# Performance work log

Hardware: AMD Instinct MI355X
Metric: run time of the kernel (lower is better)

## Reference

```python
import jax, jax.numpy as jnp
import numpy as np

B, D_IN, D_HID, D_OUT, E = 8192, 1024, 4096, 1024, 8


def setup_inputs() -> dict:
    key = jax.random.key(0)
    ks = jax.random.split(key, 6)
    s_in = 1.0 / np.sqrt(D_IN)
    s_gh = 1.0 / np.sqrt(D_HID // 2)
    s_eh = 1.0 / np.sqrt(D_HID)
    return {
        "x": jax.random.normal(ks[0], (B, D_IN), jnp.float32),
        "gW1": jax.random.normal(ks[1], (D_IN, D_HID // 2), jnp.float32) * s_in,
        "gb1": jnp.zeros((D_HID // 2,), jnp.float32),
        "gW2": jax.random.normal(ks[2], (D_HID // 2, E), jnp.float32) * s_gh,
        "gb2": jnp.zeros((E,), jnp.float32),
        "eW1": jax.random.normal(ks[3], (E, D_IN, D_HID), jnp.float32) * s_in,
        "eb1": jnp.zeros((E, D_HID), jnp.float32),
        "eW2": jax.random.normal(ks[4], (E, D_HID, D_OUT), jnp.float32) * s_eh,
        "eb2": jnp.zeros((E, D_OUT), jnp.float32),
    }


def reference(x, gW1, gb1, gW2, gb2, eW1, eb1, eW2, eb2):
    # Gating network: Linear -> ReLU -> (Dropout: eval identity) -> Linear -> Softmax(dim=1)
    gh = jax.nn.relu(x @ gW1 + gb1)                      # [B, H/2]
    gates = jax.nn.softmax(gh @ gW2 + gb2, axis=1)       # [B, E]

    # All experts run on the full batch (dense MoE): batched GEMMs over expert axis.
    h = jax.nn.relu(jnp.einsum('bi,eih->beh', x, eW1) + eb1)   # [B, E, H]
    eo = jnp.einsum('beh,eho->beo', h, eW2) + eb2              # [B, E, O]

    # Gated weighted sum over experts.
    combined = jnp.einsum('beo,be->bo', eo, gates)             # [B, O]
    return (combined, gates, gates)
```

## Files before the change

kernel.cpp:

```cpp
#include <hip/hip_runtime.h>
#include <hip/hip_bf16.h>
#include <stdint.h>

#define BB 8192
#define DIN 1024
#define DHID 4096
#define DOUT 1024
#define NEXP 8
#define GH_N 2048

typedef __attribute__((ext_vector_type(8))) __bf16 bf16x8;
typedef __attribute__((ext_vector_type(4))) float f32x4;

__device__ inline unsigned short f2bf(float f) {
  unsigned u = __builtin_bit_cast(unsigned, f);
  u = (u + 0x7FFFu + ((u >> 16) & 1u)) >> 16;
  return (unsigned short)u;
}
__device__ inline float b2f(unsigned short s) {
  return __builtin_bit_cast(float, (unsigned)s << 16);
}

__global__ void cvt_f32_bf16(const float* __restrict__ in,
                             unsigned short* __restrict__ out, int n4) {
  int i = blockIdx.x * blockDim.x + threadIdx.x;
  if (i >= n4) return;
  float4 v = ((const float4*)in)[i];
  ushort4 o;
  o.x = f2bf(v.x); o.y = f2bf(v.y); o.z = f2bf(v.z); o.w = f2bf(v.w);
  ((ushort4*)out)[i] = o;
}

__device__ inline void tr_tile(const float* __restrict__ in,
                               unsigned short* __restrict__ out, int R, int C,
                               int bx, int by) {
  __shared__ float tile[32][33];
  int c0 = bx * 32, r0 = by * 32;
  int tx = threadIdx.x & 31, ty = threadIdx.x >> 5;
#pragma unroll
  for (int i = 0; i < 4; ++i)
    tile[ty + i * 8][tx] = in[(size_t)(r0 + ty + i * 8) * C + c0 + tx];
  __syncthreads();
#pragma unroll
  for (int i = 0; i < 4; ++i)
    out[(size_t)(c0 + ty + i * 8) * R + r0 + tx] = f2bf(tile[tx][ty + i * 8]);
}

__global__ void transpose_cvt(const float* __restrict__ in,
                              unsigned short* __restrict__ out, int R, int C) {
  tr_tile(in, out, R, C, blockIdx.x, blockIdx.y);
}

__global__ void transpose_cvt2(const float* __restrict__ w1,
                               unsigned short* __restrict__ w1T,
                               const float* __restrict__ w2,
                               unsigned short* __restrict__ w2T) {
  int b = blockIdx.x;
  if (b < 4096) {
    tr_tile(w1, w1T, DIN, DHID, b & 127, b >> 7);
  } else {
    b -= 4096;
    tr_tile(w2, w2T, DHID, DOUT, b & 31, b >> 5);
  }
}

__device__ inline void gload16(const void* g, void* l) {
  __builtin_amdgcn_global_load_lds(
      (const __attribute__((address_space(1))) void*)g,
      (__attribute__((address_space(3))) void*)l, 16, 0, 0);
}

template <int N>
__device__ inline void waitv() {
  if constexpr (N == 0) asm volatile("s_waitcnt vmcnt(0)" ::: "memory");
  else if constexpr (N == 2) asm volatile("s_waitcnt vmcnt(2)" ::: "memory");
  else if constexpr (N == 4) asm volatile("s_waitcnt vmcnt(4)" ::: "memory");
  else asm volatile("s_waitcnt vmcnt(0)" ::: "memory");
}
__device__ inline void waitlgkm0() {
  asm volatile("s_waitcnt lgkmcnt(0)" ::: "memory");
  __builtin_amdgcn_sched_barrier(0);
}
__device__ inline bf16x8 ldr(const char* p) { return *(const bf16x8*)p; }

struct GArgs {
  const unsigned short* A;
  const unsigned short* Bt;
  int lda, ldb, N, K;
  const float* bias;
  unsigned short* outb;
  float* outf;
  const float* gates;
  int eidx, accum, epi, nb;
};

__device__ __forceinline__ void gemm_core(const GArgs& g, int local,
                                          char* Als, char* Bls) {
  constexpr int ABYTES = 32768, BBYTES = 32768;
  const int t = threadIdx.x;
  const int lane = t & 63;
  const int wid = t >> 6;
  const int wm = wid >> 2;
  const int wn = wid & 3;
  const int l15 = lane & 15, lg = lane >> 4;

  const int nb = g.nb;
  const int swz = (local & 7) * (nb >> 3) + (local >> 3);
  int ks = 0, tid = swz;
  if (g.epi == 2) { ks = swz & 1; tid = swz >> 1; }
  const int nbn = g.N >> 8;
  const int bn = tid % nbn, bm = tid / nbn;
  const int m0 = bm * 256, n0 = bn * 256;
  const int kbase = ks * g.K;
  float* outf = g.outf;
  if (g.epi == 2) outf += (size_t)ks * ((size_t)BB * g.N);

  const int prow = t >> 3;
  const int cOff = ((t & 7) ^ (prow & 7)) * 8;
  const unsigned short* aP[4];
  const unsigned short* bP[4];
#pragma unroll
  for (int u = 0; u < 4; ++u) {
    int p = u * 64 + prow;
    int ga = ((p >> 6) & 1) * 128 + ((p >> 7) & 1) * 64 + (p & 63);
    aP[u] = g.A + (size_t)(m0 + ga) * g.lda + kbase + cOff;
    int gb = ((p >> 5) & 3) * 64 + ((p >> 7) & 1) * 32 + (p & 31);
    bP[u] = g.Bt + (size_t)(n0 + gb) * g.ldb + kbase + cOff;
  }
  const int ldst = t * 16;

  const int slot0 = ((lg) ^ (l15 & 7)) * 16;
  const int slot1 = ((4 + lg) ^ (l15 & 7)) * 16;
  const int aRB0 = (wm * 64 + l15) * 128;
  const int aRB1 = (128 + wm * 64 + l15) * 128;
  const int bCB0 = (wn * 32 + l15) * 128;
  const int bCB1 = (128 + wn * 32 + l15) * 128;

  f32x4 acc[8][4];
  const f32x4 zero = {0.f, 0.f, 0.f, 0.f};
#pragma unroll
  for (int i = 0; i < 8; ++i)
#pragma unroll
    for (int j = 0; j < 4; ++j) acc[i][j] = zero;

  bf16x8 ar[4][2], bc0[2][2], bc1[2][2];
  const int NT = g.K >> 6;

  gload16(bP[0], Bls + 0 * 8192 + ldst);
  gload16(bP[1], Bls + 1 * 8192 + ldst);
  gload16(aP[0], Als + 0 * 8192 + ldst);
  gload16(aP[1], Als + 1 * 8192 + ldst);
  gload16(bP[2], Bls + 2 * 8192 + ldst);
  gload16(bP[3], Bls + 3 * 8192 + ldst);
  gload16(aP[2], Als + 2 * 8192 + ldst);
  gload16(aP[3], Als + 3 * 8192 + ldst);
  waitv<4>();
  __builtin_amdgcn_s_barrier();

  for (int T = 0; T < NT; ++T) {
    const int buf = T & 1;
    const char* Ab = Als + buf * ABYTES;
    const char* Bb = Bls + buf * BBYTES;
    char* An = Als + (buf ^ 1) * ABYTES;
    char* Bn = Bls + (buf ^ 1) * BBYTES;
    const bool stg = (T + 1 < NT);
    const int kn = (T + 1) << 6;

#pragma unroll
    for (int f = 0; f < 4; ++f) {
      ar[f][0] = ldr(Ab + aRB0 + f * 2048 + slot0);
      ar[f][1] = ldr(Ab + aRB0 + f * 2048 + slot1);
    }
#pragma unroll
    for (int c = 0; c < 2; ++c) {
      bc0[c][0] = ldr(Bb + bCB0 + c * 2048 + slot0);
      bc0[c][1] = ldr(Bb + bCB0 + c * 2048 + slot1);
    }
    if (stg) {
      gload16(bP[0] + kn, Bn + 0 * 8192 + ldst);
      gload16(bP[1] + kn, Bn + 1 * 8192 + ldst);
    }
    __builtin_amdgcn_s_barrier();
    waitlgkm0();
    __builtin_amdgcn_s_setprio(1);
#pragma unroll
    for (int ksl = 0; ksl < 2; ++ksl)
#pragma unroll
      for (int f = 0; f < 4; ++f)
#pragma unroll
        for (int c = 0; c < 2; ++c)
          acc[f][c] = __builtin_amdgcn_mfma_f32_16x16x32_bf16(
              ar[f][ksl], bc0[c][ksl], acc[f][c], 0, 0, 0);
    __builtin_amdgcn_s_setprio(0);
    if (stg) waitv<4>(); else waitv<2>();
    __builtin_amdgcn_s_barrier();

#pragma unroll
    for (int c = 0; c < 2; ++c) {
      bc1[c][0] = ldr(Bb + bCB1 + c * 2048 + slot0);
      bc1[c][1] = ldr(Bb + bCB1 + c * 2048 + slot1);
    }
    if (stg) {
      gload16(aP[0] + kn, An + 0 * 8192 + ldst);
      gload16(aP[1] + kn, An + 1 * 8192 + ldst);
    }
    __builtin_amdgcn_s_barrier();
    waitlgkm0();
    __builtin_amdgcn_s_setprio(1);
#pragma unroll
    for (int ksl = 0; ksl < 2; ++ksl)
#pragma unroll
      for (int f = 0; f < 4; ++f)
#pragma unroll
        for (int c = 0; c < 2; ++c)
          acc[f][2 + c] = __builtin_amdgcn_mfma_f32_16x16x32_bf16(
              ar[f][ksl], bc1[c][ksl], acc[f][2 + c], 0, 0, 0);
    __builtin_amdgcn_s_setprio(0);
    if (stg) waitv<4>(); else waitv<0>();
    __builtin_amdgcn_s_barrier();

#pragma unroll
    for (int f = 0; f < 4; ++f) {
      ar[f][0] = ldr(Ab + aRB1 + f * 2048 + slot0);
      ar[f][1] = ldr(Ab + aRB1 + f * 2048 + slot1);
    }
    if (stg) {
      gload16(bP[2] + kn, Bn + 2 * 8192 + ldst);
      gload16(bP[3] + kn, Bn + 3 * 8192 + ldst);
    }
    __builtin_amdgcn_s_barrier();
    waitlgkm0();
    __builtin_amdgcn_s_setprio(1);
#pragma unroll
    for (int ksl = 0; ksl < 2; ++ksl)
#pragma unroll
      for (int f = 0; f < 4; ++f)
#pragma unroll
        for (int c = 0; c < 2; ++c)
          acc[4 + f][2 + c] = __builtin_amdgcn_mfma_f32_16x16x32_bf16(
              ar[f][ksl], bc1[c][ksl], acc[4 + f][2 + c], 0, 0, 0);
    __builtin_amdgcn_s_setprio(0);
    __builtin_amdgcn_s_barrier();

    if (stg) {
      gload16(aP[2] + kn, An + 2 * 8192 + ldst);
      gload16(aP[3] + kn, An + 3 * 8192 + ldst);
    }
    __builtin_amdgcn_s_barrier();
    __builtin_amdgcn_s_setprio(1);
#pragma unroll
    for (int ksl = 0; ksl < 2; ++ksl)
#pragma unroll
      for (int f = 0; f < 4; ++f)
#pragma unroll
        for (int c = 0; c < 2; ++c)
          acc[4 + f][c] = __builtin_amdgcn_mfma_f32_16x16x32_bf16(
              ar[f][ksl], bc0[c][ksl], acc[4 + f][c], 0, 0, 0);
    __builtin_amdgcn_s_setprio(0);
    if (stg) waitv<4>();
    __builtin_amdgcn_s_barrier();
  }

  const int rb = m0 + wm * 128 + (lg << 2);
  const int cb = n0 + wn * 64 + l15;
  const int N = g.N;
  if (g.epi == 0) {
#pragma unroll
    for (int fg = 0; fg < 8; ++fg) {
#pragma unroll
      for (int j = 0; j < 4; ++j) {
        int col = cb + j * 16;
        float bv = g.bias[col];
#pragma unroll
        for (int r = 0; r < 4; ++r) {
          int row = rb + fg * 16 + r;
          float v = acc[fg][j][r] + bv;
          g.outb[(size_t)row * N + col] = f2bf(fmaxf(v, 0.f));
        }
      }
    }
  } else if (g.epi == 1) {
#pragma unroll
    for (int fg = 0; fg < 8; ++fg) {
      float gv[4];
#pragma unroll
      for (int r = 0; r < 4; ++r)
        gv[r] = g.gates[(size_t)(rb + fg * 16 + r) * NEXP + g.eidx];
#pragma unroll
      for (int j = 0; j < 4; ++j) {
        int col = cb + j * 16;
        float bv = g.bias[col];
#pragma unroll
        for (int r = 0; r < 4; ++r) {
          size_t o = (size_t)(rb + fg * 16 + r) * N + col;
          float v = (acc[fg][j][r] + bv) * gv[r];
          outf[o] = g.accum ? outf[o] + v : v;
        }
      }
    }
  } else {
#pragma unroll
    for (int fg = 0; fg < 8; ++fg) {
#pragma unroll
      for (int j = 0; j < 4; ++j) {
        int col = cb + j * 16;
#pragma unroll
        for (int r = 0; r < 4; ++r) {
          size_t o = (size_t)(rb + fg * 16 + r) * N + col;
          outf[o] = acc[fg][j][r];
        }
      }
    }
  }
}

__global__ __launch_bounds__(512, 2)
void gemmU(GArgs a, GArgs b, int nbA) {
  __shared__ char lds[131072];
  const bool rA = (int)blockIdx.x < nbA;
  const GArgs& sel = rA ? a : b;
  const int local = rA ? (int)blockIdx.x : (int)blockIdx.x - nbA;
  gemm_core(sel, local, lds, lds + 65536);
}

__global__ void combine_k(const float* __restrict__ p0,
                          const float* __restrict__ p1,
                          const float* __restrict__ bias,
                          const float* __restrict__ gates, int eidx,
                          float* __restrict__ outC) {
  int i = blockIdx.x * blockDim.x + threadIdx.x;
  int r = i >> 8, c4 = i & 255;
  float g = gates[(size_t)r * NEXP + eidx];
  float4 a = ((const float4*)(p0 + (size_t)r * DOUT))[c4];
  float4 b = ((const float4*)(p1 + (size_t)r * DOUT))[c4];
  float4 bb = ((const float4*)bias)[c4];
  float4 p = ((const float4*)(outC + (size_t)r * DOUT))[c4];
  float4 o;
  o.x = p.x + g * (a.x + b.x + bb.x);
  o.y = p.y + g * (a.y + b.y + bb.y);
  o.z = p.z + g * (a.z + b.z + bb.z);
  o.w = p.w + g * (a.w + b.w + bb.w);
  ((float4*)(outC + (size_t)r * DOUT))[c4] = o;
}

__global__ __launch_bounds__(512)
void gating_head2(const unsigned short* __restrict__ gh,
                  const float* __restrict__ gW2,
                  const float* __restrict__ gb2,
                  float* __restrict__ gws,
                  float* __restrict__ g1,
                  float* __restrict__ g2) {
  __shared__ float wT[8][2048];
  const int t = threadIdx.x;
  for (int idx = t; idx < 16384; idx += 512) {
    wT[idx & 7][idx >> 3] = gW2[idx];
  }
  __syncthreads();
  const int wid = t >> 6, lane = t & 63;
  const int row = blockIdx.x * 8 + wid;
  const unsigned short* ghr = gh + (size_t)row * 2048;
  float s[8] = {0.f, 0.f, 0.f, 0.f, 0.f, 0.f, 0.f, 0.f};
#pragma unroll
  for (int j = 0; j < 8; ++j) {
    int k4 = lane + 64 * j;
    ushort4 hv = ((const ushort4*)ghr)[k4];
    float h0 = b2f(hv.x), h1 = b2f(hv.y), h2 = b2f(hv.z), h3 = b2f(hv.w);
#pragma unroll
    for (int e = 0; e < 8; ++e) {
      float4 w = ((const float4*)&wT[e][0])[k4];
      s[e] += h0 * w.x + h1 * w.y + h2 * w.z + h3 * w.w;
    }
  }
#pragma unroll
  for (int e = 0; e < 8; ++e)
#pragma unroll
    for (int off = 1; off < 64; off <<= 1) s[e] += __shfl_xor(s[e], off, 64);
  if (lane == 0) {
    float l[8], m = -1e30f;
#pragma unroll
    for (int e = 0; e < 8; ++e) {
      l[e] = s[e] + gb2[e];
      m = fmaxf(m, l[e]);
    }
    float sum = 0.f;
#pragma unroll
    for (int e = 0; e < 8; ++e) {
      l[e] = expf(l[e] - m);
      sum += l[e];
    }
    float inv = 1.f / sum;
#pragma unroll
    for (int e = 0; e < 8; ++e) {
      float gv = l[e] * inv;
      gws[(size_t)row * 8 + e] = gv;
      g1[(size_t)row * 8 + e] = gv;
      g2[(size_t)row * 8 + e] = gv;
    }
  }
}

extern "C" void kernel_launch(void* const* d_in, const int* in_sizes, int n_in,
                              void* d_out, int out_size, void* d_ws,
                              size_t ws_size, hipStream_t stream) {
  (void)in_sizes; (void)n_in; (void)out_size;
  const float* x   = (const float*)d_in[0];
  const float* gW1 = (const float*)d_in[1];
  const float* gb1 = (const float*)d_in[2];
  const float* gW2 = (const float*)d_in[3];
  const float* gb2 = (const float*)d_in[4];
  const float* eW1 = (const float*)d_in[5];
  const float* eb1 = (const float*)d_in[6];
  const float* eW2 = (const float*)d_in[7];
  const float* eb2 = (const float*)d_in[8];

  float* outC  = (float*)d_out;
  float* outG1 = outC + (size_t)BB * DOUT;
  float* outG2 = outG1 + (size_t)BB * NEXP;

  char* ws = (char*)d_ws;
  unsigned short* xb    = (unsigned short*)(ws);
  float*          gat   = (float*)(ws + 16777216);
  unsigned short* w1T   = (unsigned short*)(ws + 17039360);
  unsigned short* w2T   = (unsigned short*)(ws + 25427968);
  unsigned short* hbufA = (unsigned short*)(ws + 33816576);
  unsigned short* hbufB = (unsigned short*)(ws + 100925440);
  unsigned short* gh    = hbufA;
  unsigned short* gW1T  = hbufB;
  float* p0 = (float*)hbufA;
  float* p1 = (float*)(ws + 33816576 + 33554432);
  const bool paired = ws_size >= (size_t)168034304;

  cvt_f32_bf16<<<(BB * DIN / 4) / 256, 256, 0, stream>>>(x, xb, BB * DIN / 4);
  transpose_cvt<<<dim3(GH_N / 32, DIN / 32), 256, 0, stream>>>(gW1, gW1T, DIN, GH_N);
  {
    GArgs a{xb, gW1T, DIN, DIN, GH_N, DIN, gb1, gh, nullptr, nullptr, 0, 0, 0, 256};
    gemmU<<<256, 512, 0, stream>>>(a, a, 256);
  }
  gating_head2<<<BB / 8, 512, 0, stream>>>(gh, gW2, gb2, gat, outG1, outG2);

  transpose_cvt2<<<8192, 256, 0, stream>>>(eW1, w1T, eW2, w2T);
  {
    GArgs a{xb, w1T, DIN, DIN, DHID, DIN, eb1, hbufA, nullptr, nullptr, 0, 0, 0, 512};
    gemmU<<<512, 512, 0, stream>>>(a, a, 512);
  }

  for (int e = 0; e < 7; ++e) {
    transpose_cvt<<<dim3(DHID / 32, DIN / 32), 256, 0, stream>>>(
        eW1 + (size_t)(e + 1) * DIN * DHID, w1T, DIN, DHID);
    unsigned short* hcur = (e & 1) ? hbufB : hbufA;
    unsigned short* hnxt = paired ? ((e & 1) ? hbufA : hbufB) : hbufA;
    GArgs g2{hcur, w2T, DHID, DHID, DOUT, DHID, eb2 + (size_t)e * DOUT,
             nullptr, outC, gat, e, (e > 0) ? 1 : 0, 1, 128};
    GArgs g1{xb, w1T, DIN, DIN, DHID, DIN, eb1 + (size_t)(e + 1) * DHID,
             hnxt, nullptr, nullptr, 0, 0, 0, 512};
    if (paired) {
      gemmU<<<640, 512, 0, stream>>>(g2, g1, 128);
    } else {
      g2.A = hbufA; g1.outb = hbufA;
      gemmU<<<128, 512, 0, stream>>>(g2, g2, 128);
      gemmU<<<512, 512, 0, stream>>>(g1, g1, 512);
    }
    transpose_cvt<<<dim3(DOUT / 32, DHID / 32), 256, 0, stream>>>(
        eW2 + (size_t)(e + 1) * DHID * DOUT, w2T, DHID, DOUT);
  }

  if (paired) {
    GArgs a{hbufB, w2T, DHID, DHID, DOUT, DHID / 2, nullptr, nullptr, p0,
            nullptr, 7, 0, 2, 256};
    gemmU<<<256, 512, 0, stream>>>(a, a, 256);
    combine_k<<<(BB * DOUT / 4) / 256, 256, 0, stream>>>(
        p0, p1, eb2 + (size_t)7 * DOUT, gat, 7, outC);
  } else {
    GArgs a{hbufA, w2T, DHID, DHID, DOUT, DHID, eb2 + (size_t)7 * DOUT,
            nullptr, outC, gat, 7, 1, 1, 128};
    gemmU<<<128, 512, 0, stream>>>(a, a, 128);
  }
}
```

Baseline: 1.335 ms.

## Split-K second expert GEMM with atomic accumulation; drop paired launches

Replaces the paired GEMM launches (second GEMM of expert e co-scheduled with first GEMM of expert e+1) with a simple serial per-expert sequence. The second GEMM now always uses split-K by two, and both halves atomically add gated results into the output, which is pre-initialised with the gated bias sum. The transpose tile grows from 32x32 to 64x64. This removes the separate combine kernel and the double-buffered hidden state, but gives up the inter-expert overlap and adds float atomics on the full output for every expert.

```diff
diff --git a/kernel.cpp b/kernel.cpp
--- a/kernel.cpp
+++ b/kernel.cpp
@@ -31,24 +31,28 @@
   ((ushort4*)out)[i] = o;
 }
 
-__device__ inline void tr_tile(const float* __restrict__ in,
-                               unsigned short* __restrict__ out, int R, int C,
-                               int bx, int by) {
-  __shared__ float tile[32][33];
-  int c0 = bx * 32, r0 = by * 32;
-  int tx = threadIdx.x & 31, ty = threadIdx.x >> 5;
-#pragma unroll
-  for (int i = 0; i < 4; ++i)
-    tile[ty + i * 8][tx] = in[(size_t)(r0 + ty + i * 8) * C + c0 + tx];
+__device__ inline void tr_tile64(const float* __restrict__ in,
+                                 unsigned short* __restrict__ out, int R, int C,
+                                 int bx, int by) {
+  __shared__ float tile[64][65];
+  const int c0 = bx * 64, r0 = by * 64;
+  const int tx = threadIdx.x & 63, ty = threadIdx.x >> 6;
+#pragma unroll
+  for (int i = 0; i < 16; ++i) {
+    int r = i * 4 + ty;
+    tile[r][tx] = in[(size_t)(r0 + r) * C + c0 + tx];
+  }
   __syncthreads();
 #pragma unroll
-  for (int i = 0; i < 4; ++i)
-    out[(size_t)(c0 + ty + i * 8) * R + r0 + tx] = f2bf(tile[tx][ty + i * 8]);
-}
-
-__global__ void transpose_cvt(const float* __restrict__ in,
-                              unsigned short* __restrict__ out, int R, int C) {
-  tr_tile(in, out, R, C, blockIdx.x, blockIdx.y);
+  for (int i = 0; i < 16; ++i) {
+    int r = i * 4 + ty;
+    out[(size_t)(c0 + r) * R + r0 + tx] = f2bf(tile[tx][r]);
+  }
+}
+
+__global__ void transpose_cvt64(const float* __restrict__ in,
+                                unsigned short* __restrict__ out, int R, int C) {
+  tr_tile64(in, out, R, C, blockIdx.x, blockIdx.y);
 }
 
 __global__ void transpose_cvt2(const float* __restrict__ w1,
@@ -56,11 +60,11 @@
                                const float* __restrict__ w2,
                                unsigned short* __restrict__ w2T) {
   int b = blockIdx.x;
-  if (b < 4096) {
-    tr_tile(w1, w1T, DIN, DHID, b & 127, b >> 7);
+  if (b < 1024) {
+    tr_tile64(w1, w1T, DIN, DHID, b & 63, b >> 6);
   } else {
-    b -= 4096;
-    tr_tile(w2, w2T, DHID, DOUT, b & 31, b >> 5);
+    b -= 1024;
+    tr_tile64(w2, w2T, DHID, DOUT, b & 15, b >> 4);
   }
 }
 
@@ -91,11 +95,14 @@
   unsigned short* outb;
   float* outf;
   const float* gates;
-  int eidx, accum, epi, nb;
+  int eidx, epi, nb;
 };
 
-__device__ __forceinline__ void gemm_core(const GArgs& g, int local,
-                                          char* Als, char* Bls) {
+__global__ __launch_bounds__(512, 2)
+void gemmU(GArgs g) {
+  __shared__ char lds[131072];
+  char* Als = lds;
+  char* Bls = lds + 65536;
   constexpr int ABYTES = 32768, BBYTES = 32768;
   const int t = threadIdx.x;
   const int lane = t & 63;
@@ -105,15 +112,14 @@
   const int l15 = lane & 15, lg = lane >> 4;
 
   const int nb = g.nb;
+  const int local = blockIdx.x;
   const int swz = (local & 7) * (nb >> 3) + (local >> 3);
   int ks = 0, tid = swz;
-  if (g.epi == 2) { ks = swz & 1; tid = swz >> 1; }
+  if (g.epi == 3) { ks = swz & 1; tid = swz >> 1; }
   const int nbn = g.N >> 8;
   const int bn = tid % nbn, bm = tid / nbn;
   const int m0 = bm * 256, n0 = bn * 256;
   const int kbase = ks * g.K;
-  float* outf = g.outf;
-  if (g.epi == 2) outf += (size_t)ks * ((size_t)BB * g.N);
 
   const int prow = t >> 3;
   const int cOff = ((t & 7) ^ (prow & 7)) * 8;
@@ -279,7 +285,7 @@
         }
       }
     }
-  } else if (g.epi == 1) {
+  } else {
 #pragma unroll
     for (int fg = 0; fg < 8; ++fg) {
       float gv[4];
@@ -289,57 +295,32 @@
 #pragma unroll
       for (int j = 0; j < 4; ++j) {
         int col = cb + j * 16;
-        float bv = g.bias[col];
 #pragma unroll
         for (int r = 0; r < 4; ++r) {
           size_t o = (size_t)(rb + fg * 16 + r) * N + col;
-          float v = (acc[fg][j][r] + bv) * gv[r];
-          outf[o] = g.accum ? outf[o] + v : v;
+          __hip_atomic_fetch_add(&g.outf[o], acc[fg][j][r] * gv[r],
+                                 __ATOMIC_RELAXED, __HIP_MEMORY_SCOPE_AGENT);
         }
       }
     }
-  } else {
-#pragma unroll
-    for (int fg = 0; fg < 8; ++fg) {
-#pragma unroll
-      for (int j = 0; j < 4; ++j) {
-        int col = cb + j * 16;
-#pragma unroll
-        for (int r = 0; r < 4; ++r) {
-          size_t o = (size_t)(rb + fg * 16 + r) * N + col;
-          outf[o] = acc[fg][j][r];
-        }
-      }
-    }
-  }
-}
-
-__global__ __launch_bounds__(512, 2)
-void gemmU(GArgs a, GArgs b, int nbA) {
-  __shared__ char lds[131072];
-  const bool rA = (int)blockIdx.x < nbA;
-  const GArgs& sel = rA ? a : b;
-  const int local = rA ? (int)blockIdx.x : (int)blockIdx.x - nbA;
-  gemm_core(sel, local, lds, lds + 65536);
-}
-
-__global__ void combine_k(const float* __restrict__ p0,
-                          const float* __restrict__ p1,
-                          const float* __restrict__ bias,
-                          const float* __restrict__ gates, int eidx,
-                          float* __restrict__ outC) {
-  int i = blockIdx.x * blockDim.x + threadIdx.x;
-  int r = i >> 8, c4 = i & 255;
-  float g = gates[(size_t)r * NEXP + eidx];
-  float4 a = ((const float4*)(p0 + (size_t)r * DOUT))[c4];
-  float4 b = ((const float4*)(p1 + (size_t)r * DOUT))[c4];
-  float4 bb = ((const float4*)bias)[c4];
-  float4 p = ((const float4*)(outC + (size_t)r * DOUT))[c4];
-  float4 o;
-  o.x = p.x + g * (a.x + b.x + bb.x);
-  o.y = p.y + g * (a.y + b.y + bb.y);
-  o.z = p.z + g * (a.z + b.z + bb.z);
-  o.w = p.w + g * (a.w + b.w + bb.w);
+  }
+}
+
+__global__ void init_c(const float* __restrict__ gat,
+                       const float* __restrict__ eb2,
+                       float* __restrict__ outC) {
+  const int r = blockIdx.x;
+  const int c4 = threadIdx.x;
+  float g[8];
+#pragma unroll
+  for (int e = 0; e < 8; ++e) g[e] = gat[(size_t)r * NEXP + e];
+  float4 o = {0.f, 0.f, 0.f, 0.f};
+#pragma unroll
+  for (int e = 0; e < 8; ++e) {
+    float4 b = ((const float4*)(eb2 + (size_t)e * DOUT))[c4];
+    o.x += g[e] * b.x; o.y += g[e] * b.y;
+    o.z += g[e] * b.z; o.w += g[e] * b.w;
+  }
   ((float4*)(outC + (size_t)r * DOUT))[c4] = o;
 }
 
@@ -402,7 +383,7 @@
 extern "C" void kernel_launch(void* const* d_in, const int* in_sizes, int n_in,
                               void* d_out, int out_size, void* d_ws,
                               size_t ws_size, hipStream_t stream) {
-  (void)in_sizes; (void)n_in; (void)out_size;
+  (void)in_sizes; (void)n_in; (void)out_size; (void)ws_size;
   const float* x   = (const float*)d_in[0];
   const float* gW1 = (const float*)d_in[1];
   const float* gb1 = (const float*)d_in[2];
@@ -418,61 +399,35 @@
   float* outG2 = outG1 + (size_t)BB * NEXP;
 
   char* ws = (char*)d_ws;
-  unsigned short* xb    = (unsigned short*)(ws);
-  float*          gat   = (float*)(ws + 16777216);
-  unsigned short* w1T   = (unsigned short*)(ws + 17039360);
-  unsigned short* w2T   = (unsigned short*)(ws + 25427968);
-  unsigned short* hbufA = (unsigned short*)(ws + 33816576);
-  unsigned short* hbufB = (unsigned short*)(ws + 100925440);
-  unsigned short* gh    = hbufA;
-  unsigned short* gW1T  = hbufB;
-  float* p0 = (float*)hbufA;
-  float* p1 = (float*)(ws + 33816576 + 33554432);
-  const bool paired = ws_size >= (size_t)168034304;
+  unsigned short* xb   = (unsigned short*)(ws);
+  float*          gat  = (float*)(ws + 16777216);
+  unsigned short* w1T  = (unsigned short*)(ws + 17039360);
+  unsigned short* w2T  = (unsigned short*)(ws + 25427968);
+  unsigned short* hbuf = (unsigned short*)(ws + 33816576);
+  unsigned short* gh   = hbuf;
+  unsigned short* gW1T = w1T;
 
   cvt_f32_bf16<<<(BB * DIN / 4) / 256, 256, 0, stream>>>(x, xb, BB * DIN / 4);
-  transpose_cvt<<<dim3(GH_N / 32, DIN / 32), 256, 0, stream>>>(gW1, gW1T, DIN, GH_N);
+  transpose_cvt64<<<dim3(GH_N / 64, DIN / 64), 256, 0, stream>>>(gW1, gW1T, DIN, GH_N);
   {
-    GArgs a{xb, gW1T, DIN, DIN, GH_N, DIN, gb1, gh, nullptr, nullptr, 0, 0, 0, 256};
-    gemmU<<<256, 512, 0, stream>>>(a, a, 256);
+    GArgs a{xb, gW1T, DIN, DIN, GH_N, DIN, gb1, gh, nullptr, nullptr, 0, 0, 256};
+    gemmU<<<256, 512, 0, stream>>>(a);
   }
   gating_head2<<<BB / 8, 512, 0, stream>>>(gh, gW2, gb2, gat, outG1, outG2);
-
-  transpose_cvt2<<<8192, 256, 0, stream>>>(eW1, w1T, eW2, w2T);
-  {
-    GArgs a{xb, w1T, DIN, DIN, DHID, DIN, eb1, hbufA, nullptr, nullptr, 0, 0, 0, 512};
-    gemmU<<<512, 512, 0, stream>>>(a, a, 512);
-  }
-
-  for (int e = 0; e < 7; ++e) {
-    transpose_cvt<<<dim3(DHID / 32, DIN / 32), 256, 0, stream>>>(
-        eW1 + (size_t)(e + 1) * DIN * DHID, w1T, DIN, DHID);
-    unsigned short* hcur = (e & 1) ? hbufB : hbufA;
-    unsigned short* hnxt = paired ? ((e & 1) ? hbufA : hbufB) : hbufA;
-    GArgs g2{hcur, w2T, DHID, DHID, DOUT, DHID, eb2 + (size_t)e * DOUT,
-             nullptr, outC, gat, e, (e > 0) ? 1 : 0, 1, 128};
-    GArgs g1{xb, w1T, DIN, DIN, DHID, DIN, eb1 + (size_t)(e + 1) * DHID,
-             hnxt, nullptr, nullptr, 0, 0, 0, 512};
-    if (paired) {
-      gemmU<<<640, 512, 0, stream>>>(g2, g1, 128);
-    } else {
-      g2.A = hbufA; g1.outb = hbufA;
-      gemmU<<<128, 512, 0, stream>>>(g2, g2, 128);
-      gemmU<<<512, 512, 0, stream>>>(g1, g1, 512);
-    }
-    transpose_cvt<<<dim3(DOUT / 32, DHID / 32), 256, 0, stream>>>(
-        eW2 + (size_t)(e + 1) * DHID * DOUT, w2T, DHID, DOUT);
-  }
-
-  if (paired) {
-    GArgs a{hbufB, w2T, DHID, DHID, DOUT, DHID / 2, nullptr, nullptr, p0,
-            nullptr, 7, 0, 2, 256};
-    gemmU<<<256, 512, 0, stream>>>(a, a, 256);
-    combine_k<<<(BB * DOUT / 4) / 256, 256, 0, stream>>>(
-        p0, p1, eb2 + (size_t)7 * DOUT, gat, 7, outC);
-  } else {
-    GArgs a{hbufA, w2T, DHID, DHID, DOUT, DHID, eb2 + (size_t)7 * DOUT,
-            nullptr, outC, gat, 7, 1, 1, 128};
-    gemmU<<<128, 512, 0, stream>>>(a, a, 128);
-  }
-}
+  init_c<<<BB, 256, 0, stream>>>(gat, eb2, outC);
+
+  for (int e = 0; e < NEXP; ++e) {
+    transpose_cvt2<<<2048, 256, 0, stream>>>(
+        eW1 + (size_t)e * DIN * DHID, w1T, eW2 + (size_t)e * DHID * DOUT, w2T);
+    {
+      GArgs a{xb, w1T, DIN, DIN, DHID, DIN, eb1 + (size_t)e * DHID,
+              hbuf, nullptr, nullptr, 0, 0, 512};
+      gemmU<<<512, 512, 0, stream>>>(a);
+    }
+    {
+      GArgs a{hbuf, w2T, DHID, DHID, DOUT, DHID / 2, nullptr, nullptr,
+              outC, gat, e, 3, 256};
+      gemmU<<<256, 512, 0, stream>>>(a);
+    }
+  }
+}
```

Result: slower. 1.551 ms (+16.2%).
